# Performance work log

Hardware: AMD Instinct MI355X
Metric: run time of the kernel (lower is better)

The kernel has to match this reference:

```python
import jax, jax.numpy as jnp
import numpy as np

B, N, D, STK_TOTAL = 8, 2048, 128, 4000


def setup_inputs() -> dict:
    key = jax.random.key(0)
    k1, k2, k3, k4 = jax.random.split(key, 4)
    x = jax.random.normal(k1, (B, N, D), dtype=jnp.float32)
    stk_ten = jax.random.randint(k2, (B, N), 0, STK_TOTAL, dtype=jnp.int32)
    # learned parameter tables (trained state; original inits: ones / xavier-uniform)
    stk_matrix = jax.random.normal(k3, (STK_TOTAL, STK_TOTAL), dtype=jnp.float32)
    stk_weight = jax.random.normal(k4, (STK_TOTAL, STK_TOTAL), dtype=jnp.float32)
    return {"x": x, "stk_ten": stk_ten, "stk_matrix": stk_matrix, "stk_weight": stk_weight}


def reference(x, stk_ten, stk_matrix, stk_weight):
    # x: [B, N, D]; stk_ten: [B, N] int ids < STK_TOTAL
    idx = stk_ten.astype(jnp.int32)
    # per-batch double gather -> [B, N, N] submatrices (vectorized index_select x2)
    M = stk_matrix[idx[:, :, None], idx[:, None, :]]          # [B, N, N]
    W = jnp.abs(stk_weight[idx[:, :, None], idx[:, None, :]])  # [B, N, N]
    n = idx.shape[1]
    eye = jnp.eye(n, dtype=bool)                               # diag removal mask
    M = jnp.where(eye, jnp.float32(0.0), M)                    # stk_m_s - diag_embed(diag)
    W = jnp.where(eye, jnp.float32(0.0), W)
    # dropout is identity in inference mode (training=False)
    att = jax.nn.softmax(W, axis=2)                            # [B, N, N]
    out = jnp.matmul(M * att, x)                               # [B, N, D]
    return out
```

## Files before the change

### kernel.cpp

```cpp
#include <hip/hip_runtime.h>
#include <hip/hip_fp16.h>
#include <math.h>

#define BATCH 8
#define N 2048
#define D 128
#define ST 4000

#define TJ 64
#define IT 16
#define KQ 4
#define TPW 8

typedef short bf16x8 __attribute__((ext_vector_type(8)));
typedef float f32x4  __attribute__((ext_vector_type(4)));
typedef unsigned u32x4 __attribute__((ext_vector_type(4)));

__device__ __forceinline__ unsigned short f2bf(float f) {
    union { float f; unsigned u; } v; v.f = f;
    const unsigned r = v.u + 0x7FFFu + ((v.u >> 16) & 1u);
    return (unsigned short)(r >> 16);
}

__global__ __launch_bounds__(256) void pack_kernel(
    const float* __restrict__ M, const float* __restrict__ W,
    unsigned* __restrict__ P)
{
    const size_t i4 = ((size_t)blockIdx.x * 256 + threadIdx.x) * 4;
    const f32x4 m4 = __builtin_nontemporal_load((const f32x4*)(M + i4));
    const f32x4 w4 = __builtin_nontemporal_load((const f32x4*)(W + i4));
    u32x4 o;
    {
        const float e = __expf(fabsf(w4.x));
        o.x = ((unsigned)f2bf(m4.x * e) << 16) | (unsigned)f2bf(e);
    }
    {
        const float e = __expf(fabsf(w4.y));
        o.y = ((unsigned)f2bf(m4.y * e) << 16) | (unsigned)f2bf(e);
    }
    {
        const float e = __expf(fabsf(w4.z));
        o.z = ((unsigned)f2bf(m4.z * e) << 16) | (unsigned)f2bf(e);
    }
    {
        const float e = __expf(fabsf(w4.w));
        o.w = ((unsigned)f2bf(m4.w * e) << 16) | (unsigned)f2bf(e);
    }
    *(u32x4*)(P + i4) = o;
}

__global__ __launch_bounds__(1024) void sort_kernel(
    const int* __restrict__ stk_ten,
    int* __restrict__ sval,
    int* __restrict__ spos)
{
    __shared__ int hist[4000];
    __shared__ int base[4000];
    __shared__ int wsum[16];
    const int b = blockIdx.x, t = threadIdx.x;
    const int lane = t & 63, wv = t >> 6;
    const int* idxb = stk_ten + b * N;

    for (int j = t; j < 4000; j += 1024) hist[j] = 0;
    __syncthreads();
    const int v0 = idxb[t], v1 = idxb[t + 1024];
    atomicAdd(&hist[v0], 1);
    atomicAdd(&hist[v1], 1);
    __syncthreads();

    int h[4], c[4], run = 0;
    #pragma unroll
    for (int i = 0; i < 4; ++i) {
        const int bi = 4 * t + i;
        h[i] = (bi < 4000) ? hist[bi] : 0;
        run += h[i];
        c[i] = run;
    }
    const int tsum = run;
    int incl = tsum;
    #pragma unroll
    for (int d = 1; d < 64; d <<= 1) {
        const int tmp = __shfl_up(incl, d, 64);
        if (lane >= d) incl += tmp;
    }
    if (lane == 63) wsum[wv] = incl;
    __syncthreads();
    if (t < 16) {
        const int v = wsum[t];
        int iv = v;
        #pragma unroll
        for (int d = 1; d < 16; d <<= 1) {
            const int tmp = __shfl_up(iv, d, 64);
            if (lane >= d) iv += tmp;
        }
        wsum[t] = iv - v;
    }
    __syncthreads();
    const int ex = incl - tsum + wsum[wv];
    #pragma unroll
    for (int i = 0; i < 4; ++i) {
        const int bi = 4 * t + i;
        if (bi < 4000) base[bi] = ex + c[i] - h[i];
    }
    __syncthreads();
    for (int j = t; j < 4000; j += 1024) hist[j] = 0;
    __syncthreads();
    {
        const int p0 = base[v0] + atomicAdd(&hist[v0], 1);
        sval[b * N + p0] = v0; spos[b * N + p0] = t;
        const int p1 = base[v1] + atomicAdd(&hist[v1], 1);
        sval[b * N + p1] = v1; spos[b * N + p1] = t + 1024;
    }
}

__global__ __launch_bounds__(256) void xt_kernel(
    const float* __restrict__ x,
    const int* __restrict__ spos,
    unsigned short* __restrict__ xT)
{
    __shared__ float xs[TJ][129];
    __shared__ int sp_s[TJ];
    const int t  = threadIdx.x;
    const int b  = blockIdx.x >> 5;
    const int jt = blockIdx.x & 31;
    const int j0 = jt * TJ;
    if (t < TJ) sp_s[t] = spos[b * N + j0 + t];
    __syncthreads();
    const int tx = t & 31, ty = t >> 5;
    const float* xb = x + (size_t)b * N * D;
    #pragma unroll
    for (int p = 0; p < 8; ++p) {
        const int r = ty + 8 * p;
        const float* src = xb + (size_t)sp_s[r] * D;
        #pragma unroll
        for (int i = 0; i < 4; ++i)
            xs[r][tx + 32 * i] = src[tx + 32 * i];
    }
    __syncthreads();
    const int jp = t & 31, dd0 = t >> 5;
    unsigned short* xTb = xT + (size_t)b * D * N;
    #pragma unroll
    for (int q = 0; q < 16; ++q) {
        const int dd = dd0 + 8 * q;
        const unsigned lo = f2bf(xs[2 * jp][dd]);
        const unsigned hi = f2bf(xs[2 * jp + 1][dd]);
        *(unsigned*)(xTb + (size_t)dd * N + j0 + 2 * jp) = (hi << 16) | lo;
    }
}

__global__ __launch_bounds__(256) __attribute__((amdgpu_waves_per_eu(3)))
void fused_kernel(
    const unsigned short* __restrict__ xT,
    const int* __restrict__ stk_ten,
    const unsigned* __restrict__ P,
    const int* __restrict__ sval,
    const int* __restrict__ spos,
    float* __restrict__ out)
{
    __shared__ __align__(16) unsigned short cs[KQ][IT * 72];
    __shared__ float accs[IT][132];
    __shared__ float lbuf[KQ][IT];
    __shared__ int ri_s[IT];

    const int t    = threadIdx.x;
    const int lane = t & 63;
    const int w    = t >> 6;
    const int wg   = (blockIdx.x & 7) * 128 + (blockIdx.x >> 3);
    const int b    = wg >> 7;
    const int i0   = (wg & 127) * IT;

    if (t < IT) ri_s[t] = stk_ten[b * N + i0 + t];
    for (int z = t; z < IT * 132; z += 256) (&accs[0][0])[z] = 0.0f;
    __syncthreads();

    unsigned rowbase[IT];
    #pragma unroll
    for (int m = 0; m < IT; ++m)
        rowbase[m] = (unsigned)__builtin_amdgcn_readfirstlane(ri_s[m]) * (unsigned)ST;

    const int* svb = sval + b * N;
    const int* spb = spos + b * N;
    const unsigned short* xTb = xT + (size_t)b * D * N;
    unsigned short* csw = &cs[w][0];

    f32x4 acc[8];
    #pragma unroll
    for (int nb = 0; nb < 8; ++nb)
        #pragma unroll
        for (int r = 0; r < 4; ++r) acc[nb][r] = 0.0f;
    float l_part[IT];
    #pragma unroll
    for (int m = 0; m < IT; ++m) l_part[m] = 0.0f;

    const int jbase = w * (TPW * TJ);
    const int brow  = lane & 15;
    const int bcol  = (lane >> 4) * 8;

    int cj = svb[jbase + lane];
    int pj = spb[jbase + lane];
    unsigned gv[IT];
    #pragma unroll
    for (int m = 0; m < IT; ++m) gv[m] = P[rowbase[m] + (unsigned)cj];

    for (int tt = 0; tt < TPW; ++tt) {
        const int j0  = jbase + tt * TJ;
        const int j0n = (tt == TPW - 1) ? jbase : j0 + TJ;

        const int cjn = svb[j0n + lane];
        const int pjn = spb[j0n + lane];
        uint4 bv[8];
        #pragma unroll
        for (int nb = 0; nb < 8; ++nb)
            bv[nb] = *(const uint4*)(xTb + (size_t)(nb * 16 + brow) * N + j0 + bcol);

        #pragma unroll
        for (int m = 0; m < IT; ++m) {
            const unsigned u = gv[m];
            const bool diag = (pj == i0 + m);
            l_part[m] += diag ? 1.0f : __uint_as_float(u << 16);
            csw[m * 72 + lane] = diag ? (unsigned short)0 : (unsigned short)(u >> 16);
        }

        const bf16x8 av0 = *(const bf16x8*)(csw + brow * 72 + bcol);
        const bf16x8 av1 = *(const bf16x8*)(csw + brow * 72 + 32 + bcol);

        unsigned gvn[IT];
        #pragma unroll
        for (int m = 0; m < IT; ++m) gvn[m] = P[rowbase[m] + (unsigned)cjn];

        #pragma unroll
        for (int nb = 0; nb < 8; ++nb)
            acc[nb] = __builtin_amdgcn_mfma_f32_16x16x32_bf16(
                av0, *(const bf16x8*)&bv[nb], acc[nb], 0, 0, 0);
        #pragma unroll
        for (int nb = 0; nb < 8; ++nb)
            bv[nb] = *(const uint4*)(xTb + (size_t)(nb * 16 + brow) * N + j0 + 32 + bcol);
        #pragma unroll
        for (int nb = 0; nb < 8; ++nb)
            acc[nb] = __builtin_amdgcn_mfma_f32_16x16x32_bf16(
                av1, *(const bf16x8*)&bv[nb], acc[nb], 0, 0, 0);

        #pragma unroll
        for (int m = 0; m < IT; ++m) gv[m] = gvn[m];
        cj = cjn; pj = pjn;
    }

    #pragma unroll
    for (int m = 0; m < IT; ++m) {
        float v = l_part[m];
        #pragma unroll
        for (int d = 1; d < 64; d <<= 1) v += __shfl_xor(v, d, 64);
        if (lane == 0) lbuf[w][m] = v;
    }
    #pragma unroll
    for (int nb = 0; nb < 8; ++nb)
        #pragma unroll
        for (int r = 0; r < 4; ++r)
            atomicAdd(&accs[(lane >> 4) * 4 + r][nb * 16 + (lane & 15)], acc[nb][r]);
    __syncthreads();

    #pragma unroll
    for (int rr = 0; rr < 4; ++rr) {
        const int row = 4 * w + rr;
        const float linv = 1.0f /
            (lbuf[0][row] + lbuf[1][row] + lbuf[2][row] + lbuf[3][row]);
        #pragma unroll
        for (int p = 0; p < 2; ++p) {
            const int dd = lane + 64 * p;
            out[((size_t)(b * N + i0 + row) << 7) + dd] = accs[row][dd] * linv;
        }
    }
}

extern "C" void kernel_launch(void* const* d_in, const int* in_sizes, int n_in,
                              void* d_out, int out_size, void* d_ws, size_t ws_size,
                              hipStream_t stream) {
    const float* x          = (const float*)d_in[0];
    const int*   stk_ten    = (const int*)d_in[1];
    const float* stk_matrix = (const float*)d_in[2];
    const float* stk_weight = (const float*)d_in[3];
    float* out = (float*)d_out;

    unsigned* P = (unsigned*)d_ws;
    int* sval = (int*)(P + (size_t)ST * ST);
    int* spos = sval + BATCH * N;
    unsigned short* xT = (unsigned short*)(spos + BATCH * N);

    pack_kernel<<<(ST * ST) / 1024, 256, 0, stream>>>(stk_matrix, stk_weight, P);
    sort_kernel<<<BATCH, 1024, 0, stream>>>(stk_ten, sval, spos);
    xt_kernel<<<BATCH * (N / TJ), 256, 0, stream>>>(x, spos, xT);
    fused_kernel<<<BATCH * (N / IT), 256, 0, stream>>>(
        xT, stk_ten, P, sval, spos, out);
}
```

Before: 281.0 us.

## Precompute softmax denominators per table row from id histograms, halve packed table

The softmax denominator for each row is now computed in the pack kernel as a histogram-weighted sum of exp(|W|) over table columns, using per-batch id counts from the sort kernel, minus the diagonal term plus one. The packed table shrinks from 32-bit (M*e, e) pairs to 16-bit M*e only. This halves the gather traffic in the fused kernel and removes its per-row denominator accumulation and reductions. In exchange, the pack kernel does more arithmetic and reads counts per column, and it must now run after the sort kernel. It also drops the waves_per_eu hint.

Result: slower. 293.0 us (+4.3%).

```diff
diff --git a/kernel.cpp b/kernel.cpp
--- a/kernel.cpp
+++ b/kernel.cpp
@@ -14,7 +14,7 @@
 
 typedef short bf16x8 __attribute__((ext_vector_type(8)));
 typedef float f32x4  __attribute__((ext_vector_type(4)));
-typedef unsigned u32x4 __attribute__((ext_vector_type(4)));
+typedef unsigned short u16x4 __attribute__((ext_vector_type(4)));
 
 __device__ __forceinline__ unsigned short f2bf(float f) {
     union { float f; unsigned u; } v; v.f = f;
@@ -22,37 +22,11 @@
     return (unsigned short)(r >> 16);
 }
 
-__global__ __launch_bounds__(256) void pack_kernel(
-    const float* __restrict__ M, const float* __restrict__ W,
-    unsigned* __restrict__ P)
-{
-    const size_t i4 = ((size_t)blockIdx.x * 256 + threadIdx.x) * 4;
-    const f32x4 m4 = __builtin_nontemporal_load((const f32x4*)(M + i4));
-    const f32x4 w4 = __builtin_nontemporal_load((const f32x4*)(W + i4));
-    u32x4 o;
-    {
-        const float e = __expf(fabsf(w4.x));
-        o.x = ((unsigned)f2bf(m4.x * e) << 16) | (unsigned)f2bf(e);
-    }
-    {
-        const float e = __expf(fabsf(w4.y));
-        o.y = ((unsigned)f2bf(m4.y * e) << 16) | (unsigned)f2bf(e);
-    }
-    {
-        const float e = __expf(fabsf(w4.z));
-        o.z = ((unsigned)f2bf(m4.z * e) << 16) | (unsigned)f2bf(e);
-    }
-    {
-        const float e = __expf(fabsf(w4.w));
-        o.w = ((unsigned)f2bf(m4.w * e) << 16) | (unsigned)f2bf(e);
-    }
-    *(u32x4*)(P + i4) = o;
-}
-
 __global__ __launch_bounds__(1024) void sort_kernel(
     const int* __restrict__ stk_ten,
     int* __restrict__ sval,
-    int* __restrict__ spos)
+    int* __restrict__ spos,
+    unsigned short* __restrict__ cntT)
 {
     __shared__ int hist[4000];
     __shared__ int base[4000];
@@ -68,6 +42,8 @@
     atomicAdd(&hist[v1], 1);
     __syncthreads();
 
+    for (int j = t; j < 4000; j += 1024) cntT[(size_t)j * 8 + b] = (unsigned short)hist[j];
+
     int h[4], c[4], run = 0;
     #pragma unroll
     for (int i = 0; i < 4; ++i) {
@@ -110,6 +86,62 @@
         sval[b * N + p0] = v0; spos[b * N + p0] = t;
         const int p1 = base[v1] + atomicAdd(&hist[v1], 1);
         sval[b * N + p1] = v1; spos[b * N + p1] = t + 1024;
+    }
+}
+
+__global__ __launch_bounds__(256) void pack_kernel(
+    const float* __restrict__ M, const float* __restrict__ W,
+    const unsigned short* __restrict__ cntT,
+    unsigned short* __restrict__ P2,
+    float* __restrict__ Lb)
+{
+    __shared__ float redL[4][8];
+    __shared__ float ediag_s;
+    const int r = blockIdx.x;
+    const int t = threadIdx.x;
+    const int lane = t & 63, wv = t >> 6;
+    const size_t rowo = (size_t)r * ST;
+
+    float acc8[8];
+    #pragma unroll
+    for (int b = 0; b < 8; ++b) acc8[b] = 0.0f;
+
+    for (int it = 0; it < 4; ++it) {
+        const int c4 = (t + 256 * it) * 4;
+        if (c4 < ST) {
+            const f32x4 m4 = __builtin_nontemporal_load((const f32x4*)(M + rowo + c4));
+            const f32x4 w4 = __builtin_nontemporal_load((const f32x4*)(W + rowo + c4));
+            u16x4 o;
+            #pragma unroll
+            for (int k = 0; k < 4; ++k) {
+                const float e = __expf(fabsf(w4[k]));
+                o[k] = f2bf(m4[k] * e);
+                if (c4 + k == r) ediag_s = e;
+                const uint4 cv = *(const uint4*)(cntT + (size_t)(c4 + k) * 8);
+                acc8[0] += (float)(cv.x & 0xFFFFu) * e;
+                acc8[1] += (float)(cv.x >> 16)     * e;
+                acc8[2] += (float)(cv.y & 0xFFFFu) * e;
+                acc8[3] += (float)(cv.y >> 16)     * e;
+                acc8[4] += (float)(cv.z & 0xFFFFu) * e;
+                acc8[5] += (float)(cv.z >> 16)     * e;
+                acc8[6] += (float)(cv.w & 0xFFFFu) * e;
+                acc8[7] += (float)(cv.w >> 16)     * e;
+            }
+            *(u16x4*)(P2 + rowo + c4) = o;
+        }
+    }
+
+    #pragma unroll
+    for (int b = 0; b < 8; ++b) {
+        float v = acc8[b];
+        #pragma unroll
+        for (int d = 1; d < 64; d <<= 1) v += __shfl_xor(v, d, 64);
+        if (lane == 0) redL[wv][b] = v;
+    }
+    __syncthreads();
+    if (t < 8) {
+        const float s = redL[0][t] + redL[1][t] + redL[2][t] + redL[3][t];
+        Lb[(size_t)t * ST + r] = s - ediag_s + 1.0f;
     }
 }
 
@@ -148,18 +180,17 @@
     }
 }
 
-__global__ __launch_bounds__(256) __attribute__((amdgpu_waves_per_eu(3)))
-void fused_kernel(
+__global__ __launch_bounds__(256) void fused_kernel(
     const unsigned short* __restrict__ xT,
     const int* __restrict__ stk_ten,
-    const unsigned* __restrict__ P,
+    const unsigned short* __restrict__ P2,
     const int* __restrict__ sval,
     const int* __restrict__ spos,
+    const float* __restrict__ Lb,
     float* __restrict__ out)
 {
     __shared__ __align__(16) unsigned short cs[KQ][IT * 72];
     __shared__ float accs[IT][132];
-    __shared__ float lbuf[KQ][IT];
     __shared__ int ri_s[IT];
 
     const int t    = threadIdx.x;
@@ -175,8 +206,7 @@
 
     unsigned rowbase[IT];
     #pragma unroll
-    for (int m = 0; m < IT; ++m)
-        rowbase[m] = (unsigned)__builtin_amdgcn_readfirstlane(ri_s[m]) * (unsigned)ST;
+    for (int m = 0; m < IT; ++m) rowbase[m] = (unsigned)ri_s[m] * ST;
 
     const int* svb = sval + b * N;
     const int* spb = spos + b * N;
@@ -188,9 +218,6 @@
     for (int nb = 0; nb < 8; ++nb)
         #pragma unroll
         for (int r = 0; r < 4; ++r) acc[nb][r] = 0.0f;
-    float l_part[IT];
-    #pragma unroll
-    for (int m = 0; m < IT; ++m) l_part[m] = 0.0f;
 
     const int jbase = w * (TPW * TJ);
     const int brow  = lane & 15;
@@ -200,7 +227,7 @@
     int pj = spb[jbase + lane];
     unsigned gv[IT];
     #pragma unroll
-    for (int m = 0; m < IT; ++m) gv[m] = P[rowbase[m] + (unsigned)cj];
+    for (int m = 0; m < IT; ++m) gv[m] = P2[rowbase[m] + (unsigned)cj];
 
     for (int tt = 0; tt < TPW; ++tt) {
         const int j0  = jbase + tt * TJ;
@@ -215,10 +242,8 @@
 
         #pragma unroll
         for (int m = 0; m < IT; ++m) {
-            const unsigned u = gv[m];
             const bool diag = (pj == i0 + m);
-            l_part[m] += diag ? 1.0f : __uint_as_float(u << 16);
-            csw[m * 72 + lane] = diag ? (unsigned short)0 : (unsigned short)(u >> 16);
+            csw[m * 72 + lane] = diag ? (unsigned short)0 : (unsigned short)gv[m];
         }
 
         const bf16x8 av0 = *(const bf16x8*)(csw + brow * 72 + bcol);
@@ -226,7 +251,7 @@
 
         unsigned gvn[IT];
         #pragma unroll
-        for (int m = 0; m < IT; ++m) gvn[m] = P[rowbase[m] + (unsigned)cjn];
+        for (int m = 0; m < IT; ++m) gvn[m] = P2[rowbase[m] + (unsigned)cjn];
 
         #pragma unroll
         for (int nb = 0; nb < 8; ++nb)
@@ -246,13 +271,6 @@
     }
 
     #pragma unroll
-    for (int m = 0; m < IT; ++m) {
-        float v = l_part[m];
-        #pragma unroll
-        for (int d = 1; d < 64; d <<= 1) v += __shfl_xor(v, d, 64);
-        if (lane == 0) lbuf[w][m] = v;
-    }
-    #pragma unroll
     for (int nb = 0; nb < 8; ++nb)
         #pragma unroll
         for (int r = 0; r < 4; ++r)
@@ -262,8 +280,7 @@
     #pragma unroll
     for (int rr = 0; rr < 4; ++rr) {
         const int row = 4 * w + rr;
-        const float linv = 1.0f /
-            (lbuf[0][row] + lbuf[1][row] + lbuf[2][row] + lbuf[3][row]);
+        const float linv = 1.0f / Lb[(size_t)b * ST + ri_s[row]];
         #pragma unroll
         for (int p = 0; p < 2; ++p) {
             const int dd = lane + 64 * p;
@@ -281,14 +298,16 @@
     const float* stk_weight = (const float*)d_in[3];
     float* out = (float*)d_out;
 
-    unsigned* P = (unsigned*)d_ws;
-    int* sval = (int*)(P + (size_t)ST * ST);
+    unsigned short* P2 = (unsigned short*)d_ws;
+    int* sval = (int*)(P2 + (size_t)ST * ST);
     int* spos = sval + BATCH * N;
-    unsigned short* xT = (unsigned short*)(spos + BATCH * N);
-
-    pack_kernel<<<(ST * ST) / 1024, 256, 0, stream>>>(stk_matrix, stk_weight, P);
-    sort_kernel<<<BATCH, 1024, 0, stream>>>(stk_ten, sval, spos);
+    unsigned short* cntT = (unsigned short*)(spos + BATCH * N);
+    float* Lb = (float*)(cntT + ST * 8);
+    unsigned short* xT = (unsigned short*)(Lb + BATCH * ST);
+
+    sort_kernel<<<BATCH, 1024, 0, stream>>>(stk_ten, sval, spos, cntT);
     xt_kernel<<<BATCH * (N / TJ), 256, 0, stream>>>(x, spos, xT);
+    pack_kernel<<<ST, 256, 0, stream>>>(stk_matrix, stk_weight, cntT, P2, Lb);
     fused_kernel<<<BATCH * (N / IT), 256, 0, stream>>>(
-        xT, stk_ten, P, sval, spos, out);
-}
+        xT, stk_ten, P2, sval, spos, Lb, out);
+}
```

## Stage gathered P values through LDS with async global_load_lds double buffering

Applied to the files above, without the earlier changes.

Replaces the register-held prefetch of gathered P entries with asynchronous global-to-LDS loads into a per-wave double buffer, so the scattered gather for the next tile overlaps the current tile's compute. A manual vmcnt wait and sched barrier order the loads. All x tile loads are now issued up front, and the waves_per_eu hint is removed. This adds LDS use and depends on a hand-picked vmcnt count being correct. It also removes the wave-uniform readfirstlane on the row offsets.

Measured after the change: 285.3 us. No clear change (+1.5%).

```diff
diff --git a/kernel.cpp b/kernel.cpp
--- a/kernel.cpp
+++ b/kernel.cpp
@@ -148,8 +148,7 @@
     }
 }
 
-__global__ __launch_bounds__(256) __attribute__((amdgpu_waves_per_eu(3)))
-void fused_kernel(
+__global__ __launch_bounds__(256) void fused_kernel(
     const unsigned short* __restrict__ xT,
     const int* __restrict__ stk_ten,
     const unsigned* __restrict__ P,
@@ -158,6 +157,7 @@
     float* __restrict__ out)
 {
     __shared__ __align__(16) unsigned short cs[KQ][IT * 72];
+    __shared__ __align__(16) unsigned pg[KQ][2][IT * 64];
     __shared__ float accs[IT][132];
     __shared__ float lbuf[KQ][IT];
     __shared__ int ri_s[IT];
@@ -173,15 +173,15 @@
     for (int z = t; z < IT * 132; z += 256) (&accs[0][0])[z] = 0.0f;
     __syncthreads();
 
-    unsigned rowbase[IT];
-    #pragma unroll
-    for (int m = 0; m < IT; ++m)
-        rowbase[m] = (unsigned)__builtin_amdgcn_readfirstlane(ri_s[m]) * (unsigned)ST;
+    unsigned rowoff[IT];
+    #pragma unroll
+    for (int m = 0; m < IT; ++m) rowoff[m] = (unsigned)ri_s[m] * ST;
 
     const int* svb = sval + b * N;
     const int* spb = spos + b * N;
     const unsigned short* xTb = xT + (size_t)b * D * N;
     unsigned short* csw = &cs[w][0];
+    unsigned* pgw = &pg[w][0][0];
 
     f32x4 acc[8];
     #pragma unroll
@@ -196,26 +196,48 @@
     const int brow  = lane & 15;
     const int bcol  = (lane >> 4) * 8;
 
-    int cj = svb[jbase + lane];
-    int pj = spb[jbase + lane];
-    unsigned gv[IT];
-    #pragma unroll
-    for (int m = 0; m < IT; ++m) gv[m] = P[rowbase[m] + (unsigned)cj];
-
+    int pj  = spb[jbase + lane];
+    int cjn = svb[jbase + TJ + lane];
+    int pjn = spb[jbase + TJ + lane];
+    {
+        const int cj0 = svb[jbase + lane];
+        #pragma unroll
+        for (int m = 0; m < IT; ++m)
+            __builtin_amdgcn_global_load_lds(
+                (const unsigned*)(P + rowoff[m] + (unsigned)cj0),
+                pgw + m * 64, 4, 0, 0);
+    }
+
+    int buf = 0;
     for (int tt = 0; tt < TPW; ++tt) {
-        const int j0  = jbase + tt * TJ;
-        const int j0n = (tt == TPW - 1) ? jbase : j0 + TJ;
-
-        const int cjn = svb[j0n + lane];
-        const int pjn = spb[j0n + lane];
-        uint4 bv[8];
+        const int j0 = jbase + tt * TJ;
+        const int j2 = (tt + 2 < TPW) ? j0 + 2 * TJ : jbase;
+
+        uint4 bv0[8], bv1[8];
         #pragma unroll
         for (int nb = 0; nb < 8; ++nb)
-            bv[nb] = *(const uint4*)(xTb + (size_t)(nb * 16 + brow) * N + j0 + bcol);
-
+            bv0[nb] = *(const uint4*)(xTb + (size_t)(nb * 16 + brow) * N + j0 + bcol);
+        #pragma unroll
+        for (int nb = 0; nb < 8; ++nb)
+            bv1[nb] = *(const uint4*)(xTb + (size_t)(nb * 16 + brow) * N + j0 + 32 + bcol);
+
+        unsigned* pgn = pgw + (buf ^ 1) * (IT * 64);
+        #pragma unroll
+        for (int m = 0; m < IT; ++m)
+            __builtin_amdgcn_global_load_lds(
+                (const unsigned*)(P + rowoff[m] + (unsigned)cjn),
+                pgn + m * 64, 4, 0, 0);
+
+        asm volatile("s_waitcnt vmcnt(32)" ::: "memory");
+        __builtin_amdgcn_sched_barrier(0);
+
+        const int cj2 = svb[j2 + lane];
+        const int pj2 = spb[j2 + lane];
+
+        const unsigned* pgr = pgw + buf * (IT * 64);
         #pragma unroll
         for (int m = 0; m < IT; ++m) {
-            const unsigned u = gv[m];
+            const unsigned u = pgr[m * 64 + lane];
             const bool diag = (pj == i0 + m);
             l_part[m] += diag ? 1.0f : __uint_as_float(u << 16);
             csw[m * 72 + lane] = diag ? (unsigned short)0 : (unsigned short)(u >> 16);
@@ -224,25 +246,16 @@
         const bf16x8 av0 = *(const bf16x8*)(csw + brow * 72 + bcol);
         const bf16x8 av1 = *(const bf16x8*)(csw + brow * 72 + 32 + bcol);
 
-        unsigned gvn[IT];
-        #pragma unroll
-        for (int m = 0; m < IT; ++m) gvn[m] = P[rowbase[m] + (unsigned)cjn];
-
         #pragma unroll
         for (int nb = 0; nb < 8; ++nb)
             acc[nb] = __builtin_amdgcn_mfma_f32_16x16x32_bf16(
-                av0, *(const bf16x8*)&bv[nb], acc[nb], 0, 0, 0);
-        #pragma unroll
-        for (int nb = 0; nb < 8; ++nb)
-            bv[nb] = *(const uint4*)(xTb + (size_t)(nb * 16 + brow) * N + j0 + 32 + bcol);
+                av0, *(const bf16x8*)&bv0[nb], acc[nb], 0, 0, 0);
         #pragma unroll
         for (int nb = 0; nb < 8; ++nb)
             acc[nb] = __builtin_amdgcn_mfma_f32_16x16x32_bf16(
-                av1, *(const bf16x8*)&bv[nb], acc[nb], 0, 0, 0);
-
-        #pragma unroll
-        for (int m = 0; m < IT; ++m) gv[m] = gvn[m];
-        cj = cjn; pj = pjn;
+                av1, *(const bf16x8*)&bv1[nb], acc[nb], 0, 0, 0);
+
+        buf ^= 1; pj = pjn; cjn = cj2; pjn = pj2;
     }
 
     #pragma unroll
```
